# Kernel tuning notes

Hardware: AMD Instinct MI355X
Metric: run time of the kernel (lower is better)

The kernel has to match this reference:

```python
import jax, jax.numpy as jnp
import numpy as np

H = 15  # hidden_dim


def _lstm_layer(x_seq, w_ih, w_hh, b_ih, b_hh):
    """One LSTM layer, PyTorch gate order (i, f, g, o).
    x_seq: (T, B, D_in) -> returns output sequence (T, B, H)."""
    T, B, _ = x_seq.shape
    # Precompute input contribution for all timesteps at once: (T, B, 4H)
    xw = jnp.einsum('tbd,gd->tbg', x_seq, w_ih) + b_ih + b_hh

    def step(carry, xw_t):
        h, c = carry
        gates = xw_t + h @ w_hh.T  # (B, 4H)
        i, f, g, o = jnp.split(gates, 4, axis=-1)
        i = jax.nn.sigmoid(i)
        f = jax.nn.sigmoid(f)
        g = jnp.tanh(g)
        o = jax.nn.sigmoid(o)
        c = f * c + i * g
        h = o * jnp.tanh(c)
        return (h, c), h

    h0 = jnp.zeros((B, H), dtype=x_seq.dtype)
    c0 = jnp.zeros((B, H), dtype=x_seq.dtype)
    _, out = jax.lax.scan(step, (h0, c0), xw)
    return out  # (T, B, H)


def setup_inputs() -> dict:
    key = jax.random.key(0)
    ks = jax.random.split(key, 11)
    D, OUT = 5, 25
    s = 0.1
    return {
        'x':     jax.random.normal(ks[0], (512, 4096, D), dtype=jnp.float32),
        'w_ih0': jax.random.normal(ks[1], (4 * H, D), dtype=jnp.float32) * s,
        'w_hh0': jax.random.normal(ks[2], (4 * H, H), dtype=jnp.float32) * s,
        'b_ih0': jax.random.normal(ks[3], (4 * H,), dtype=jnp.float32) * s,
        'b_hh0': jax.random.normal(ks[4], (4 * H,), dtype=jnp.float32) * s,
        'w_ih1': jax.random.normal(ks[5], (4 * H, H), dtype=jnp.float32) * s,
        'w_hh1': jax.random.normal(ks[6], (4 * H, H), dtype=jnp.float32) * s,
        'b_ih1': jax.random.normal(ks[7], (4 * H,), dtype=jnp.float32) * s,
        'b_hh1': jax.random.normal(ks[8], (4 * H,), dtype=jnp.float32) * s,
        'w_lin': jax.random.normal(ks[9], (OUT, H), dtype=jnp.float32) * s,
        'b_lin': jax.random.normal(ks[10], (OUT,), dtype=jnp.float32) * s,
    }


def reference(x, w_ih0, w_hh0, b_ih0, b_hh0, w_ih1, w_hh1, b_ih1, b_hh1, w_lin, b_lin):
    out0 = _lstm_layer(x, w_ih0, w_hh0, b_ih0, b_hh0)      # (T, B, H)
    out1 = _lstm_layer(out0, w_ih1, w_hh1, b_ih1, b_hh1)   # (T, B, H)
    # Faithful to the source: output[:, -1, :] with seq-first layout selects
    # the last BATCH element across all timesteps -> (T, H)
    last = out1[:, -1, :]
    return last @ w_lin.T + b_lin  # (T, OUT)
```

## Files before the change

kernel.cpp:

```cpp
#include <hip/hip_runtime.h>

#define T_SEQ 512
#define BATCH 4096
#define D_IN  5
#define H     15
#define G4    60
#define OUTN  25
#define NITER (T_SEQ + 4)

#define M_SIG  (-1.4426950408889634f)
#define M_TANH (-2.8853901f)

__device__ __forceinline__ float fast_exp2(float x) {
#if __has_builtin(__builtin_amdgcn_exp2f)
  return __builtin_amdgcn_exp2f(x);
#else
  return exp2f(x);
#endif
}

__device__ __forceinline__ float fast_rcp(float x) {
#if __has_builtin(__builtin_amdgcn_rcpf)
  return __builtin_amdgcn_rcpf(x);
#else
  return 1.0f / x;
#endif
}

__device__ __forceinline__ float rl(float v, int lane) {
  return __int_as_float(__builtin_amdgcn_readlane(__float_as_int(v), lane));
}

template <int K>
__device__ __forceinline__ float qbcast(float v) {
  return __int_as_float(__builtin_amdgcn_update_dpp(
      0, __float_as_int(v), K * 0x55, 0xF, 0xF, true));
}

__device__ __forceinline__ void wg_barrier() {
  asm volatile("s_waitcnt lgkmcnt(0)" ::: "memory");
  __builtin_amdgcn_s_barrier();
  asm volatile("" ::: "memory");
}

__global__ void precompute_xw0(const float* __restrict__ x,
                               const float* __restrict__ w_ih0,
                               const float* __restrict__ b_ih0,
                               const float* __restrict__ b_hh0,
                               float* __restrict__ xw0) {
  int idx = blockIdx.x * blockDim.x + threadIdx.x;
  if (idx >= T_SEQ * G4) return;
  int t = idx / G4;
  int g = idx - t * G4;
  const float* xp = x + ((size_t)t * BATCH + (BATCH - 1)) * D_IN;
  float a = b_ih0[g] + b_hh0[g];
#pragma unroll
  for (int d = 0; d < D_IN; ++d) a = fmaf(xp[d], w_ih0[g * D_IN + d], a);
  float m = (g / H == 2) ? M_TANH : M_SIG;
  xw0[idx] = a * m;
}

__global__ void __launch_bounds__(192, 1)
lstm_pipe(const float* __restrict__ xw0,
          const float* __restrict__ w_hh0,
          const float* __restrict__ w_ih1,
          const float* __restrict__ w_hh1,
          const float* __restrict__ b_ih1,
          const float* __restrict__ b_hh1,
          const float* __restrict__ w_lin,
          const float* __restrict__ b_lin,
          float* __restrict__ out) {
  __shared__ __align__(16) float h0buf[4][16];
  __shared__ __align__(16) float h1buf[4][16];

  const int tid  = threadIdx.x;
  const int wid  = tid >> 6;
  const int lane = tid & 63;
  const int ty = lane & 3;
  const int j  = lane >> 2;
  const int g  = (j < H) ? (ty * H + j) : 0;

  const bool  isT  = (ty == 2);
  const float m    = isT ? M_TANH : M_SIG;
  const float scv  = isT ? (2.0f * M_TANH) : 1.0f;
  const float offv = isT ? (-M_TANH) : 0.0f;

  if (wid == 0) {
    float w0[H];
#pragma unroll
    for (int k = 0; k < H; ++k) w0[k] = w_hh0[g * H + k] * m;
    float sh0[H];
#pragma unroll
    for (int k = 0; k < H; ++k) sh0[k] = 0.0f;
    float c0 = 0.0f;
    float xw_cur = xw0[g];
    float xw_n1  = xw0[G4 + g];

    for (int i = 0; i < NITER; ++i) {
      if (i < T_SEQ) {
        int tn = (i + 2 < T_SEQ) ? (i + 2) : 0;
        float xw_n2 = xw0[tn * G4 + g];

        float a0 = xw_cur, a1 = 0.0f, a2 = 0.0f;
#pragma unroll
        for (int k = 0; k < 5; ++k)   a0 = fmaf(w0[k], sh0[k], a0);
#pragma unroll
        for (int k = 5; k < 10; ++k)  a1 = fmaf(w0[k], sh0[k], a1);
#pragma unroll
        for (int k = 10; k < 15; ++k) a2 = fmaf(w0[k], sh0[k], a2);
        float a = a0 + (a1 + a2);
        float e = fast_exp2(a);
        float s = fast_rcp(1.0f + e);
        float v = fmaf(s, scv, offv);
        float vi = qbcast<0>(v), vf = qbcast<1>(v), vg = qbcast<2>(v), vo = qbcast<3>(v);
        c0 = fmaf(vf, c0, vi * vg);
        float th = fmaf(fast_rcp(1.0f + fast_exp2(c0)), 2.0f, -1.0f);
        float h0v = vo * th;

        if (ty == 0 && j < H) h0buf[i & 3][j] = h0v;
#pragma unroll
        for (int k = 0; k < H; ++k) sh0[k] = rl(h0v, 4 * k);

        xw_cur = xw_n1;
        xw_n1  = xw_n2;
      }
      wg_barrier();
    }
  } else if (wid == 1) {
    float wi1[H], wh1[H];
#pragma unroll
    for (int k = 0; k < H; ++k) {
      wi1[k] = w_ih1[g * H + k] * m;
      wh1[k] = w_hh1[g * H + k] * m;
    }
    const float bias1 = (b_ih1[g] + b_hh1[g]) * m;
    float sh1[H];
#pragma unroll
    for (int k = 0; k < H; ++k) sh1[k] = 0.0f;
    float c1 = 0.0f;
    float4 hA = {0,0,0,0}, hB = {0,0,0,0}, hC = {0,0,0,0}, hD = {0,0,0,0};
    float4 nA = {0,0,0,0}, nB = {0,0,0,0}, nC = {0,0,0,0}, nD = {0,0,0,0};

    for (int i = 0; i < NITER; ++i) {
      int t1 = i - 2;
      if (0 <= t1 && t1 < T_SEQ) {
        float u0 = bias1, u1 = 0.0f, u2 = 0.0f, u3 = 0.0f, u4 = 0.0f, u5 = 0.0f;
        u0 = fmaf(wi1[0],  hA.x, u0); u0 = fmaf(wi1[1],  hA.y, u0);
        u0 = fmaf(wi1[2],  hA.z, u0); u0 = fmaf(wi1[3],  hA.w, u0);
        u0 = fmaf(wi1[4],  hB.x, u0);
        u1 = fmaf(wi1[5],  hB.y, u1); u1 = fmaf(wi1[6],  hB.z, u1);
        u1 = fmaf(wi1[7],  hB.w, u1); u1 = fmaf(wi1[8],  hC.x, u1);
        u1 = fmaf(wi1[9],  hC.y, u1);
        u2 = fmaf(wi1[10], hC.z, u2); u2 = fmaf(wi1[11], hC.w, u2);
        u2 = fmaf(wi1[12], hD.x, u2); u2 = fmaf(wi1[13], hD.y, u2);
        u2 = fmaf(wi1[14], hD.z, u2);
#pragma unroll
        for (int k = 0; k < 5; ++k)   u3 = fmaf(wh1[k], sh1[k], u3);
#pragma unroll
        for (int k = 5; k < 10; ++k)  u4 = fmaf(wh1[k], sh1[k], u4);
#pragma unroll
        for (int k = 10; k < 15; ++k) u5 = fmaf(wh1[k], sh1[k], u5);
        float b = ((u0 + u1) + (u2 + u3)) + (u4 + u5);

        float e = fast_exp2(b);
        float s = fast_rcp(1.0f + e);
        float v = fmaf(s, scv, offv);
        float qi = qbcast<0>(v), qf = qbcast<1>(v), qg = qbcast<2>(v), qo = qbcast<3>(v);
        c1 = fmaf(qf, c1, qi * qg);
        float th = fmaf(fast_rcp(1.0f + fast_exp2(c1)), 2.0f, -1.0f);
        float h1v = qo * th;

        if (ty == 0 && j < H) h1buf[t1 & 3][j] = h1v;
#pragma unroll
        for (int k = 0; k < H; ++k) sh1[k] = rl(h1v, 4 * k);
      }
      if (i - 1 >= 0 && i - 1 < T_SEQ) {
        const float4* p = (const float4*)(&h0buf[(i - 1) & 3][0]);
        nA = p[0]; nB = p[1]; nC = p[2]; nD = p[3];
      }
      wg_barrier();
      hA = nA; hB = nB; hC = nC; hD = nD;
    }
  } else {
    const int o = (lane < OUTN) ? lane : 0;
    float wl[H];
#pragma unroll
    for (int k = 0; k < H; ++k) wl[k] = w_lin[o * H + k];
    const float bl = b_lin[o];
    float4 hA = {0,0,0,0}, hB = {0,0,0,0}, hC = {0,0,0,0}, hD = {0,0,0,0};
    float4 nA = {0,0,0,0}, nB = {0,0,0,0}, nC = {0,0,0,0}, nD = {0,0,0,0};

    for (int i = 0; i < NITER; ++i) {
      int t2 = i - 4;
      if (0 <= t2) {
        float o0 = bl, o1 = 0.0f, o2 = 0.0f;
        o0 = fmaf(wl[0],  hA.x, o0); o0 = fmaf(wl[1],  hA.y, o0);
        o0 = fmaf(wl[2],  hA.z, o0); o0 = fmaf(wl[3],  hA.w, o0);
        o0 = fmaf(wl[4],  hB.x, o0);
        o1 = fmaf(wl[5],  hB.y, o1); o1 = fmaf(wl[6],  hB.z, o1);
        o1 = fmaf(wl[7],  hB.w, o1); o1 = fmaf(wl[8],  hC.x, o1);
        o1 = fmaf(wl[9],  hC.y, o1);
        o2 = fmaf(wl[10], hC.z, o2); o2 = fmaf(wl[11], hC.w, o2);
        o2 = fmaf(wl[12], hD.x, o2); o2 = fmaf(wl[13], hD.y, o2);
        o2 = fmaf(wl[14], hD.z, o2);
        if (lane < OUTN) out[t2 * OUTN + lane] = o0 + (o1 + o2);
      }
      if (i - 3 >= 0 && i - 3 < T_SEQ) {
        const float4* p = (const float4*)(&h1buf[(i - 3) & 3][0]);
        nA = p[0]; nB = p[1]; nC = p[2]; nD = p[3];
      }
      wg_barrier();
      hA = nA; hB = nB; hC = nC; hD = nD;
    }
  }
}

extern "C" void kernel_launch(void* const* d_in, const int* in_sizes, int n_in,
                              void* d_out, int out_size, void* d_ws, size_t ws_size,
                              hipStream_t stream) {
  const float* x     = (const float*)d_in[0];
  const float* w_ih0 = (const float*)d_in[1];
  const float* w_hh0 = (const float*)d_in[2];
  const float* b_ih0 = (const float*)d_in[3];
  const float* b_hh0 = (const float*)d_in[4];
  const float* w_ih1 = (const float*)d_in[5];
  const float* w_hh1 = (const float*)d_in[6];
  const float* b_ih1 = (const float*)d_in[7];
  const float* b_hh1 = (const float*)d_in[8];
  const float* w_lin = (const float*)d_in[9];
  const float* b_lin = (const float*)d_in[10];
  float* out = (float*)d_out;
  float* xw0 = (float*)d_ws;

  precompute_xw0<<<dim3((T_SEQ * G4 + 255) / 256), dim3(256), 0, stream>>>(
      x, w_ih0, b_ih0, b_hh0, xw0);
  lstm_pipe<<<dim3(1), dim3(192), 0, stream>>>(
      xw0, w_hh0, w_ih1, w_hh1, b_ih1, b_hh1, w_lin, b_lin, out);
}
```

Before: 241.6 us.

## Replace per-step barriers with tagged LDS flags and move output projection to separate kernel

Result: slower. 248.2 us (+2.7%).

```diff
diff --git a/kernel.cpp b/kernel.cpp
--- a/kernel.cpp
+++ b/kernel.cpp
@@ -6,7 +6,9 @@
 #define H     15
 #define G4    60
 #define OUTN  25
-#define NITER (T_SEQ + 4)
+#define XW_BYTES (T_SEQ * G4 * 4)
+#define H1_BYTES (T_SEQ * 16 * 4)
+#define TAG_BASE 0x5A000000
 
 #define M_SIG  (-1.4426950408889634f)
 #define M_TANH (-2.8853901f)
@@ -18,7 +20,6 @@
   return exp2f(x);
 #endif
 }
-
 __device__ __forceinline__ float fast_rcp(float x) {
 #if __has_builtin(__builtin_amdgcn_rcpf)
   return __builtin_amdgcn_rcpf(x);
@@ -26,21 +27,13 @@
   return 1.0f / x;
 #endif
 }
-
 __device__ __forceinline__ float rl(float v, int lane) {
   return __int_as_float(__builtin_amdgcn_readlane(__float_as_int(v), lane));
 }
-
 template <int K>
 __device__ __forceinline__ float qbcast(float v) {
   return __int_as_float(__builtin_amdgcn_update_dpp(
       0, __float_as_int(v), K * 0x55, 0xF, 0xF, true));
-}
-
-__device__ __forceinline__ void wg_barrier() {
-  asm volatile("s_waitcnt lgkmcnt(0)" ::: "memory");
-  __builtin_amdgcn_s_barrier();
-  asm volatile("" ::: "memory");
 }
 
 __global__ void precompute_xw0(const float* __restrict__ x,
@@ -60,18 +53,18 @@
   xw0[idx] = a * m;
 }
 
-__global__ void __launch_bounds__(192, 1)
-lstm_pipe(const float* __restrict__ xw0,
-          const float* __restrict__ w_hh0,
-          const float* __restrict__ w_ih1,
-          const float* __restrict__ w_hh1,
-          const float* __restrict__ b_ih1,
-          const float* __restrict__ b_hh1,
-          const float* __restrict__ w_lin,
-          const float* __restrict__ b_lin,
-          float* __restrict__ out) {
-  __shared__ __align__(16) float h0buf[4][16];
-  __shared__ __align__(16) float h1buf[4][16];
+__global__ void __launch_bounds__(128, 1)
+lstm_pipe2(const float* __restrict__ xw0,
+           const float* __restrict__ w_hh0,
+           const float* __restrict__ w_ih1,
+           const float* __restrict__ w_hh1,
+           const float* __restrict__ b_ih1,
+           const float* __restrict__ b_hh1,
+           const float* __restrict__ w_lin,
+           const float* __restrict__ b_lin,
+           float* __restrict__ out,
+           float* __restrict__ h1g) {
+  __shared__ __align__(16) float h0buf[T_SEQ][16];
 
   const int tid  = threadIdx.x;
   const int wid  = tid >> 6;
@@ -85,6 +78,9 @@
   const float scv  = isT ? (2.0f * M_TANH) : 1.0f;
   const float offv = isT ? (-M_TANH) : 0.0f;
 
+  for (int t = tid; t < T_SEQ; t += 128) h0buf[t][15] = 0.0f;
+  __syncthreads();
+
   if (wid == 0) {
     float w0[H];
 #pragma unroll
@@ -96,37 +92,37 @@
     float xw_cur = xw0[g];
     float xw_n1  = xw0[G4 + g];
 
-    for (int i = 0; i < NITER; ++i) {
-      if (i < T_SEQ) {
-        int tn = (i + 2 < T_SEQ) ? (i + 2) : 0;
-        float xw_n2 = xw0[tn * G4 + g];
-
-        float a0 = xw_cur, a1 = 0.0f, a2 = 0.0f;
-#pragma unroll
-        for (int k = 0; k < 5; ++k)   a0 = fmaf(w0[k], sh0[k], a0);
-#pragma unroll
-        for (int k = 5; k < 10; ++k)  a1 = fmaf(w0[k], sh0[k], a1);
-#pragma unroll
-        for (int k = 10; k < 15; ++k) a2 = fmaf(w0[k], sh0[k], a2);
-        float a = a0 + (a1 + a2);
-        float e = fast_exp2(a);
-        float s = fast_rcp(1.0f + e);
-        float v = fmaf(s, scv, offv);
-        float vi = qbcast<0>(v), vf = qbcast<1>(v), vg = qbcast<2>(v), vo = qbcast<3>(v);
-        c0 = fmaf(vf, c0, vi * vg);
-        float th = fmaf(fast_rcp(1.0f + fast_exp2(c0)), 2.0f, -1.0f);
-        float h0v = vo * th;
-
-        if (ty == 0 && j < H) h0buf[i & 3][j] = h0v;
-#pragma unroll
-        for (int k = 0; k < H; ++k) sh0[k] = rl(h0v, 4 * k);
-
-        xw_cur = xw_n1;
-        xw_n1  = xw_n2;
-      }
-      wg_barrier();
-    }
-  } else if (wid == 1) {
+    for (int t = 0; t < T_SEQ; ++t) {
+      int tn = (t + 2 < T_SEQ) ? (t + 2) : 0;
+      float xw_n2 = xw0[tn * G4 + g];
+
+      float a0 = xw_cur, a1 = 0.0f, a2 = 0.0f;
+#pragma unroll
+      for (int k = 0; k < 5; ++k)   a0 = fmaf(w0[k], sh0[k], a0);
+#pragma unroll
+      for (int k = 5; k < 10; ++k)  a1 = fmaf(w0[k], sh0[k], a1);
+#pragma unroll
+      for (int k = 10; k < 15; ++k) a2 = fmaf(w0[k], sh0[k], a2);
+      float a = a0 + (a1 + a2);
+      float e = fast_exp2(a);
+      float s = fast_rcp(1.0f + e);
+      float v = fmaf(s, scv, offv);
+      float vi = qbcast<0>(v), vf = qbcast<1>(v), vg = qbcast<2>(v), vo = qbcast<3>(v);
+      c0 = fmaf(vf, c0, vi * vg);
+      float th = fmaf(fast_rcp(1.0f + fast_exp2(c0)), 2.0f, -1.0f);
+      float h0v = vo * th;
+
+      h0buf[t][j] = h0v;
+      asm volatile("" ::: "memory");
+      h0buf[t][15] = __int_as_float(TAG_BASE + t);
+
+#pragma unroll
+      for (int k = 0; k < H; ++k) sh0[k] = rl(h0v, 4 * k);
+
+      xw_cur = xw_n1;
+      xw_n1  = xw_n2;
+    }
+  } else {
     float wi1[H], wh1[H];
 #pragma unroll
     for (int k = 0; k < H; ++k) {
@@ -134,85 +130,106 @@
       wh1[k] = w_hh1[g * H + k] * m;
     }
     const float bias1 = (b_ih1[g] + b_hh1[g]) * m;
+    float wl[H];
+    {
+      int o = (lane < OUTN) ? lane : 0;
+#pragma unroll
+      for (int k = 0; k < H; ++k) wl[k] = w_lin[o * H + k];
+    }
+    const float bl = b_lin[(lane < OUTN) ? lane : 0];
+
     float sh1[H];
 #pragma unroll
     for (int k = 0; k < H; ++k) sh1[k] = 0.0f;
     float c1 = 0.0f;
-    float4 hA = {0,0,0,0}, hB = {0,0,0,0}, hC = {0,0,0,0}, hD = {0,0,0,0};
-    float4 nA = {0,0,0,0}, nB = {0,0,0,0}, nC = {0,0,0,0}, nD = {0,0,0,0};
-
-    for (int i = 0; i < NITER; ++i) {
-      int t1 = i - 2;
-      if (0 <= t1 && t1 < T_SEQ) {
-        float u0 = bias1, u1 = 0.0f, u2 = 0.0f, u3 = 0.0f, u4 = 0.0f, u5 = 0.0f;
-        u0 = fmaf(wi1[0],  hA.x, u0); u0 = fmaf(wi1[1],  hA.y, u0);
-        u0 = fmaf(wi1[2],  hA.z, u0); u0 = fmaf(wi1[3],  hA.w, u0);
-        u0 = fmaf(wi1[4],  hB.x, u0);
-        u1 = fmaf(wi1[5],  hB.y, u1); u1 = fmaf(wi1[6],  hB.z, u1);
-        u1 = fmaf(wi1[7],  hB.w, u1); u1 = fmaf(wi1[8],  hC.x, u1);
-        u1 = fmaf(wi1[9],  hC.y, u1);
-        u2 = fmaf(wi1[10], hC.z, u2); u2 = fmaf(wi1[11], hC.w, u2);
-        u2 = fmaf(wi1[12], hD.x, u2); u2 = fmaf(wi1[13], hD.y, u2);
-        u2 = fmaf(wi1[14], hD.z, u2);
-#pragma unroll
-        for (int k = 0; k < 5; ++k)   u3 = fmaf(wh1[k], sh1[k], u3);
-#pragma unroll
-        for (int k = 5; k < 10; ++k)  u4 = fmaf(wh1[k], sh1[k], u4);
-#pragma unroll
-        for (int k = 10; k < 15; ++k) u5 = fmaf(wh1[k], sh1[k], u5);
-        float b = ((u0 + u1) + (u2 + u3)) + (u4 + u5);
-
-        float e = fast_exp2(b);
-        float s = fast_rcp(1.0f + e);
-        float v = fmaf(s, scv, offv);
-        float qi = qbcast<0>(v), qf = qbcast<1>(v), qg = qbcast<2>(v), qo = qbcast<3>(v);
-        c1 = fmaf(qf, c1, qi * qg);
-        float th = fmaf(fast_rcp(1.0f + fast_exp2(c1)), 2.0f, -1.0f);
-        float h1v = qo * th;
-
-        if (ty == 0 && j < H) h1buf[t1 & 3][j] = h1v;
-#pragma unroll
-        for (int k = 0; k < H; ++k) sh1[k] = rl(h1v, 4 * k);
+
+    float4 n0 = {0,0,0,0}, n1 = {0,0,0,0}, n2 = {0,0,0,0}, n3 = {0,0,0,0};
+
+    for (int t = 0; t < T_SEQ; ++t) {
+      float4 b0_ = n0, b1_ = n1, b2_ = n2, b3_ = n3;
+      const int want = TAG_BASE + t;
+      if (__float_as_int(b3_.w) != want) {
+        volatile const float* vt = &h0buf[t][15];
+        int guard = 0;
+        while (__float_as_int(*vt) != want && ++guard < (1 << 22)) {}
+        asm volatile("" ::: "memory");
+        const float4* p = (const float4*)&h0buf[t][0];
+        b3_ = p[3];
+        asm volatile("" ::: "memory");
+        b0_ = p[0]; b1_ = p[1]; b2_ = p[2];
       }
-      if (i - 1 >= 0 && i - 1 < T_SEQ) {
-        const float4* p = (const float4*)(&h0buf[(i - 1) & 3][0]);
-        nA = p[0]; nB = p[1]; nC = p[2]; nD = p[3];
+      if (t + 1 < T_SEQ) {
+        const float4* p = (const float4*)&h0buf[t + 1][0];
+        n3 = p[3];
+        asm volatile("" ::: "memory");
+        n0 = p[0]; n1 = p[1]; n2 = p[2];
       }
-      wg_barrier();
-      hA = nA; hB = nB; hC = nC; hD = nD;
-    }
-  } else {
-    const int o = (lane < OUTN) ? lane : 0;
-    float wl[H];
-#pragma unroll
-    for (int k = 0; k < H; ++k) wl[k] = w_lin[o * H + k];
-    const float bl = b_lin[o];
-    float4 hA = {0,0,0,0}, hB = {0,0,0,0}, hC = {0,0,0,0}, hD = {0,0,0,0};
-    float4 nA = {0,0,0,0}, nB = {0,0,0,0}, nC = {0,0,0,0}, nD = {0,0,0,0};
-
-    for (int i = 0; i < NITER; ++i) {
-      int t2 = i - 4;
-      if (0 <= t2) {
+
+      float u0 = bias1, u1 = 0.0f, u2 = 0.0f, u3 = 0.0f, u4 = 0.0f, u5 = 0.0f;
+      u0 = fmaf(wi1[0],  b0_.x, u0); u0 = fmaf(wi1[1],  b0_.y, u0);
+      u0 = fmaf(wi1[2],  b0_.z, u0); u0 = fmaf(wi1[3],  b0_.w, u0);
+      u0 = fmaf(wi1[4],  b1_.x, u0);
+      u1 = fmaf(wi1[5],  b1_.y, u1); u1 = fmaf(wi1[6],  b1_.z, u1);
+      u1 = fmaf(wi1[7],  b1_.w, u1); u1 = fmaf(wi1[8],  b2_.x, u1);
+      u1 = fmaf(wi1[9],  b2_.y, u1);
+      u2 = fmaf(wi1[10], b2_.z, u2); u2 = fmaf(wi1[11], b2_.w, u2);
+      u2 = fmaf(wi1[12], b3_.x, u2); u2 = fmaf(wi1[13], b3_.y, u2);
+      u2 = fmaf(wi1[14], b3_.z, u2);
+#pragma unroll
+      for (int k = 0; k < 5; ++k)   u3 = fmaf(wh1[k], sh1[k], u3);
+#pragma unroll
+      for (int k = 5; k < 10; ++k)  u4 = fmaf(wh1[k], sh1[k], u4);
+#pragma unroll
+      for (int k = 10; k < 15; ++k) u5 = fmaf(wh1[k], sh1[k], u5);
+      float b = ((u0 + u1) + (u2 + u3)) + (u4 + u5);
+
+      float e = fast_exp2(b);
+      float s = fast_rcp(1.0f + e);
+      float v = fmaf(s, scv, offv);
+      float qi = qbcast<0>(v), qf = qbcast<1>(v), qg = qbcast<2>(v), qo = qbcast<3>(v);
+      c1 = fmaf(qf, c1, qi * qg);
+      float th = fmaf(fast_rcp(1.0f + fast_exp2(c1)), 2.0f, -1.0f);
+      float h1v = qo * th;
+
+#pragma unroll
+      for (int k = 0; k < H; ++k) sh1[k] = rl(h1v, 4 * k);
+
+      if (h1g) {
+        h1g[t * 16 + j] = h1v;
+      } else {
         float o0 = bl, o1 = 0.0f, o2 = 0.0f;
-        o0 = fmaf(wl[0],  hA.x, o0); o0 = fmaf(wl[1],  hA.y, o0);
-        o0 = fmaf(wl[2],  hA.z, o0); o0 = fmaf(wl[3],  hA.w, o0);
-        o0 = fmaf(wl[4],  hB.x, o0);
-        o1 = fmaf(wl[5],  hB.y, o1); o1 = fmaf(wl[6],  hB.z, o1);
-        o1 = fmaf(wl[7],  hB.w, o1); o1 = fmaf(wl[8],  hC.x, o1);
-        o1 = fmaf(wl[9],  hC.y, o1);
-        o2 = fmaf(wl[10], hC.z, o2); o2 = fmaf(wl[11], hC.w, o2);
-        o2 = fmaf(wl[12], hD.x, o2); o2 = fmaf(wl[13], hD.y, o2);
-        o2 = fmaf(wl[14], hD.z, o2);
-        if (lane < OUTN) out[t2 * OUTN + lane] = o0 + (o1 + o2);
+#pragma unroll
+        for (int k = 0; k < 5; ++k)   o0 = fmaf(wl[k], sh1[k], o0);
+#pragma unroll
+        for (int k = 5; k < 10; ++k)  o1 = fmaf(wl[k], sh1[k], o1);
+#pragma unroll
+        for (int k = 10; k < 15; ++k) o2 = fmaf(wl[k], sh1[k], o2);
+        if (lane < OUTN) out[t * OUTN + lane] = o0 + (o1 + o2);
       }
-      if (i - 3 >= 0 && i - 3 < T_SEQ) {
-        const float4* p = (const float4*)(&h1buf[(i - 3) & 3][0]);
-        nA = p[0]; nB = p[1]; nC = p[2]; nD = p[3];
-      }
-      wg_barrier();
-      hA = nA; hB = nB; hC = nC; hD = nD;
     }
   }
+}
+
+__global__ void __launch_bounds__(64, 1)
+lin_out(const float* __restrict__ h1g,
+        const float* __restrict__ w_lin,
+        const float* __restrict__ b_lin,
+        float* __restrict__ out) {
+  const int t = blockIdx.x;
+  const int o = threadIdx.x;
+  if (o >= OUTN) return;
+  const float* hp = h1g + t * 16;
+  float wl[H];
+#pragma unroll
+  for (int k = 0; k < H; ++k) wl[k] = w_lin[o * H + k];
+  float o0 = b_lin[o], o1 = 0.0f, o2 = 0.0f;
+#pragma unroll
+  for (int k = 0; k < 5; ++k)   o0 = fmaf(wl[k], hp[k], o0);
+#pragma unroll
+  for (int k = 5; k < 10; ++k)  o1 = fmaf(wl[k], hp[k], o1);
+#pragma unroll
+  for (int k = 10; k < 15; ++k) o2 = fmaf(wl[k], hp[k], o2);
+  out[t * OUTN + o] = o0 + (o1 + o2);
 }
 
 extern "C" void kernel_launch(void* const* d_in, const int* in_sizes, int n_in,
@@ -232,8 +249,14 @@
   float* out = (float*)d_out;
   float* xw0 = (float*)d_ws;
 
+  float* h1g = nullptr;
+  if (ws_size >= (size_t)XW_BYTES + (size_t)H1_BYTES)
+    h1g = (float*)((char*)d_ws + XW_BYTES);
+
   precompute_xw0<<<dim3((T_SEQ * G4 + 255) / 256), dim3(256), 0, stream>>>(
       x, w_ih0, b_ih0, b_hh0, xw0);
-  lstm_pipe<<<dim3(1), dim3(192), 0, stream>>>(
-      xw0, w_hh0, w_ih1, w_hh1, b_ih1, b_hh1, w_lin, b_lin, out);
-}
+  lstm_pipe2<<<dim3(1), dim3(128), 0, stream>>>(
+      xw0, w_hh0, w_ih1, w_hh1, b_ih1, b_hh1, w_lin, b_lin, out, h1g);
+  if (h1g)
+    lin_out<<<dim3(T_SEQ), dim3(64), 0, stream>>>(h1g, w_lin, b_lin, out);
+}
```
